# Performance work log

Measured on AMD Instinct MI355X. Metric: run time of the kernel, lower is better.

## Reference

```python
import jax, jax.numpy as jnp
import numpy as np

B, T, C, H, HS = 128, 256, 384, 6, 64
DFF = 4 * C
EPS = 1e-5


def layer_norm(x, g, b):
    mu = jnp.mean(x, axis=-1, keepdims=True)
    var = jnp.mean(jnp.square(x - mu), axis=-1, keepdims=True)
    return (x - mu) * jax.lax.rsqrt(var + EPS) * g + b


def setup_inputs() -> dict:
    key = jax.random.key(0)
    ks = jax.random.split(key, 12)
    s_in = 1.0 / np.sqrt(C)
    s_ff = 1.0 / np.sqrt(DFF)
    return {
        "x": jax.random.normal(ks[0], (B, T, C), jnp.float32),
        "Wq": jax.random.normal(ks[1], (H, C, HS), jnp.float32) * s_in,
        "Wk": jax.random.normal(ks[2], (H, C, HS), jnp.float32) * s_in,
        "Wv": jax.random.normal(ks[3], (H, C, HS), jnp.float32) * s_in,
        "Wo": jax.random.normal(ks[4], (C, C), jnp.float32) * s_in,
        "bo": jnp.zeros((C,), jnp.float32),
        "W1": jax.random.normal(ks[5], (C, DFF), jnp.float32) * s_in,
        "b1": jnp.zeros((DFF,), jnp.float32),
        "W2": jax.random.normal(ks[6], (DFF, C), jnp.float32) * s_ff,
        "b2": jnp.zeros((C,), jnp.float32),
        "g1": jnp.ones((C,), jnp.float32),
        "be1": jnp.zeros((C,), jnp.float32),
        "g2": jnp.ones((C,), jnp.float32),
        "be2": jnp.zeros((C,), jnp.float32),
    }


def reference(x, Wq, Wk, Wv, Wo, bo, W1, b1, W2, b2, g1, be1, g2, be2):
    # --- pre-norm causal multi-head self-attention (dropout = identity, eval mode) ---
    h = layer_norm(x, g1, be1)                      # (B,T,C)
    q = jnp.einsum('btc,hcd->bhtd', h, Wq)          # (B,H,T,HS)
    k = jnp.einsum('btc,hcd->bhtd', h, Wk)
    v = jnp.einsum('btc,hcd->bhtd', h, Wv)
    scale = HS ** -0.5
    wei = jnp.einsum('bhtd,bhsd->bhts', q, k) * scale   # (B,H,T,T)
    causal = jnp.tril(jnp.ones((T, T), bool))
    wei = jnp.where(causal, wei, -jnp.inf)
    wei = jax.nn.softmax(wei, axis=-1)
    attn = jnp.einsum('bhts,bhsd->bhtd', wei, v)         # (B,H,T,HS)
    attn = attn.transpose(0, 2, 1, 3).reshape(x.shape[0], x.shape[1], C)  # concat heads
    sa = attn @ Wo + bo
    x = x + sa
    # --- pre-norm FFN ---
    h2 = layer_norm(x, g2, be2)
    ff = jax.nn.relu(h2 @ W1 + b1) @ W2 + b2
    return x + ff
```

## Files before the change

### kernel.cpp

```cpp
#include <hip/hip_runtime.h>
#include <hip/hip_bf16.h>

#define BB   128
#define TT   256
#define CC   384
#define HH   6
#define HSZ  64
#define DFF  1536
#define EPSV 1e-5f
#define RPB  8
#define NTOK (BB * TT)
#define NQKV (3 * CC)

typedef __attribute__((ext_vector_type(8))) short  short8;
typedef __attribute__((ext_vector_type(4))) float  f32x4;
typedef __hip_bfloat16 bf16;

__device__ __forceinline__ void async_copy16(const bf16* g, bf16* l) {
    __builtin_amdgcn_global_load_lds(
        (const __attribute__((address_space(1))) void*)g,
        (__attribute__((address_space(3))) void*)l, 16, 0, 0);
}

__device__ __forceinline__ void block_reduce2(float& a, float& b, float* red) {
    #pragma unroll
    for (int off = 32; off > 0; off >>= 1) {
        a += __shfl_down(a, off, 64);
        b += __shfl_down(b, off, 64);
    }
    const int lane = threadIdx.x & 63;
    const int wid  = threadIdx.x >> 6;
    if (lane == 0) { red[wid * 2] = a; red[wid * 2 + 1] = b; }
    __syncthreads();
    if (threadIdx.x == 0) {
        float sa = 0.f, sb = 0.f;
        #pragma unroll
        for (int w = 0; w < 6; ++w) { sa += red[w * 2]; sb += red[w * 2 + 1]; }
        red[12] = sa; red[13] = sb;
    }
    __syncthreads();
    a = red[12]; b = red[13];
}

__global__ __launch_bounds__(CC) void ln_bf16_kernel(
        const float* __restrict__ x, const float* __restrict__ g,
        const float* __restrict__ be, bf16* __restrict__ y) {
    __shared__ float red[16];
    const int tid = threadIdx.x;
    const long row0 = (long)blockIdx.x * RPB;
    const float gg = g[tid], bb = be[tid];
    for (int r = 0; r < RPB; ++r) {
        float v = x[(row0 + r) * CC + tid];
        float s = v, sq = v * v;
        block_reduce2(s, sq, red);
        float mu  = s  * (1.0f / CC);
        float var = sq * (1.0f / CC) - mu * mu;
        float rs  = rsqrtf(var + EPSV);
        y[(row0 + r) * CC + tid] = __float2bfloat16((v - mu) * rs * gg + bb);
        __syncthreads();
    }
}

__global__ __launch_bounds__(256) void pack_weights(
        const float* __restrict__ Wq, const float* __restrict__ Wk,
        const float* __restrict__ Wv, const float* __restrict__ Wo,
        const float* __restrict__ W1, const float* __restrict__ W2,
        bf16* __restrict__ WcatT, bf16* __restrict__ WoT,
        bf16* __restrict__ W1T, bf16* __restrict__ W2T) {
    __shared__ float t[32][33];
    const int id = blockIdx.x;
    const float* in; bf16* out; int R, Cn, c0, r0;
    if (id < 432) {
        const int which = id / 144, rem = id % 144, h = rem / 24, tt = rem % 24;
        const float* W = (which == 0) ? Wq : ((which == 1) ? Wk : Wv);
        in = W + (long)h * CC * HSZ;  R = CC; Cn = HSZ;
        c0 = (tt % 2) * 32; r0 = (tt / 2) * 32;
        out = WcatT + ((long)which * CC + h * HSZ) * CC;
    } else if (id < 576) {
        const int i2 = id - 432;
        in = Wo; out = WoT; R = CC; Cn = CC;
        c0 = (i2 % 12) * 32; r0 = (i2 / 12) * 32;
    } else if (id < 1152) {
        const int i3 = id - 576;
        in = W1; out = W1T; R = CC; Cn = DFF;
        c0 = (i3 % 48) * 32; r0 = (i3 / 48) * 32;
    } else {
        const int i4 = id - 1152;
        in = W2; out = W2T; R = DFF; Cn = CC;
        c0 = (i4 % 12) * 32; r0 = (i4 / 12) * 32;
    }
    const int tid = threadIdx.x, tx = tid & 31, ty = tid >> 5;
    #pragma unroll
    for (int p = 0; p < 4; ++p)
        t[ty + p * 8][tx] = in[(long)(r0 + ty + p * 8) * Cn + c0 + tx];
    __syncthreads();
    #pragma unroll
    for (int p = 0; p < 4; ++p)
        out[(long)(c0 + ty + p * 8) * R + r0 + tx] = __float2bfloat16(t[tx][ty + p * 8]);
}

template<int K, int EPI>
__global__ __launch_bounds__(256) void gemm_bt(
        const bf16* __restrict__ A, const bf16* __restrict__ BT,
        const float* __restrict__ bias, const float* __restrict__ res,
        float* __restrict__ outF, bf16* __restrict__ outB, int N, int nby) {
    __shared__ bf16 As[2][128 * 32];
    __shared__ bf16 Bs[2][128 * 32];

    const int tid = threadIdx.x;

    const int hwid  = blockIdx.x;
    const int chunk = gridDim.x >> 3;
    const int e     = hwid & 7;
    const int s     = hwid >> 3;
    const int gx    = chunk / nby;
    const int bx    = e * gx + s / nby;
    const int by    = s - (s / nby) * nby;
    const int m0 = bx * 128;
    const int n0 = by * 128;

    const int ln   = tid & 63;
    const int wid  = tid >> 6;
    const int wm   = (wid & 1) * 64;
    const int wn   = (wid >> 1) * 64;
    const int fr   = ln & 15;
    const int quad = ln >> 4;
    const int slot = quad ^ ((fr >> 1) & 3);

    const int u0 = tid, u1 = tid + 256;
    const int r0c = u0 >> 2, g0 = (u0 & 3) ^ ((r0c >> 1) & 3);
    const int r1c = u1 >> 2, g1 = (u1 & 3) ^ ((r1c >> 1) & 3);
    const long ga0 = (long)r0c * K + g0 * 8;
    const long ga1 = (long)r1c * K + g1 * 8;
    const bf16* Ap  = A  + (long)m0 * K;
    const bf16* BTp = BT + (long)n0 * K;

    f32x4 acc[4][4];
    #pragma unroll
    for (int i = 0; i < 4; ++i)
        #pragma unroll
        for (int j = 0; j < 4; ++j)
            acc[i][j] = (f32x4){0.f, 0.f, 0.f, 0.f};

    constexpr int NT = K / 32;

    async_copy16(Ap  + ga0, As[0] + u0 * 8);
    async_copy16(Ap  + ga1, As[0] + u1 * 8);
    async_copy16(BTp + ga0, Bs[0] + u0 * 8);
    async_copy16(BTp + ga1, Bs[0] + u1 * 8);
    __syncthreads();

    int cur = 0;
    for (int t = 0; t < NT; ++t) {
        if (t + 1 < NT) {
            const int nxt = cur ^ 1;
            const long k0 = (long)(t + 1) * 32;
            async_copy16(Ap  + ga0 + k0, As[nxt] + u0 * 8);
            async_copy16(Ap  + ga1 + k0, As[nxt] + u1 * 8);
            async_copy16(BTp + ga0 + k0, Bs[nxt] + u0 * 8);
            async_copy16(BTp + ga1 + k0, Bs[nxt] + u1 * 8);
        }
        short8 af[4], bfr[4];
        #pragma unroll
        for (int i = 0; i < 4; ++i) {
            const int R = wm + i * 16 + fr;
            af[i] = *(const short8*)(As[cur] + R * 32 + slot * 8);
        }
        #pragma unroll
        for (int j = 0; j < 4; ++j) {
            const int R = wn + j * 16 + fr;
            bfr[j] = *(const short8*)(Bs[cur] + R * 32 + slot * 8);
        }
        #pragma unroll
        for (int i = 0; i < 4; ++i)
            #pragma unroll
            for (int j = 0; j < 4; ++j)
                acc[i][j] = __builtin_amdgcn_mfma_f32_16x16x32_bf16(
                    af[i], bfr[j], acc[i][j], 0, 0, 0);
        __syncthreads();
        cur ^= 1;
    }

    #pragma unroll
    for (int i = 0; i < 4; ++i) {
        #pragma unroll
        for (int j = 0; j < 4; ++j) {
            const int col = n0 + wn + j * 16 + fr;
            #pragma unroll
            for (int r = 0; r < 4; ++r) {
                const int row = m0 + wm + i * 16 + quad * 4 + r;
                const long idx = (long)row * N + col;
                float v = acc[i][j][r];
                if (EPI == 1) {
                    v = fmaxf(v + bias[col], 0.f);
                    outB[idx] = __float2bfloat16(v);
                } else if (EPI == 2) {
                    outF[idx] = v + bias[col] + res[idx];
                } else {
                    outB[idx] = __float2bfloat16(v);
                }
            }
        }
    }
}

struct alignas(8) bh4s { bf16 a, b, c, d; };

__global__ __launch_bounds__(256, 2) void attn_mfma_kernel(
        const bf16* __restrict__ qkv, bf16* __restrict__ ab) {
    __shared__ bf16 Kt[64][72];
    __shared__ bf16 Vt[64][72];
    __shared__ bf16 Pb[4][16][72];

    const int tid  = threadIdx.x;
    const int bh   = blockIdx.x;
    const int b    = bh / HH, h = bh % HH;
    const int w    = tid >> 6;
    const int ln   = tid & 63;
    const int ln15 = ln & 15;
    const int quad = ln >> 4;

    short8 qf[4][2];
    #pragma unroll
    for (int i = 0; i < 4; ++i) {
        const long tok = (long)b * TT + w * 16 + i * 64 + ln15;
        const bf16* p = qkv + tok * NQKV + h * HSZ + quad * 8;
        qf[i][0] = *(const short8*)p;
        qf[i][1] = *(const short8*)(p + 32);
    }

    f32x4 accO[4][4];
    float mrow[4][4], lrow[4][4];
    #pragma unroll
    for (int i = 0; i < 4; ++i) {
        #pragma unroll
        for (int j = 0; j < 4; ++j) accO[i][j] = (f32x4){0.f, 0.f, 0.f, 0.f};
        #pragma unroll
        for (int r = 0; r < 4; ++r) { mrow[i][r] = -1e30f; lrow[i][r] = 0.f; }
    }

    for (int sidx = 0; sidx < 4; ++sidx) {
        const int s0 = sidx * 64;
        __syncthreads();
        {
            const bf16* kg = qkv + (long)(b * TT + s0) * NQKV + CC + h * HSZ;
            #pragma unroll
            for (int it = 0; it < 2; ++it) {
                const int u = tid + it * 256;
                const int r = u >> 3, c = (u & 7) * 8;
                *(uint4*)&Kt[r][c] = *(const uint4*)(kg + (long)r * NQKV + c);
            }
            const bf16* vg = qkv + (long)(b * TT + s0) * NQKV + 2 * CC + h * HSZ;
            const int s = tid & 63;
            #pragma unroll
            for (int it = 0; it < 4; ++it) {
                const int dq = (tid >> 6) + it * 4;
                const bh4s vv = *(const bh4s*)(vg + (long)s * NQKV + dq * 4);
                Vt[dq * 4 + 0][s] = vv.a;
                Vt[dq * 4 + 1][s] = vv.b;
                Vt[dq * 4 + 2][s] = vv.c;
                Vt[dq * 4 + 3][s] = vv.d;
            }
        }
        __syncthreads();

        #pragma unroll
        for (int i = 0; i < 4; ++i) {
            if (i < sidx) continue;
            const int rb = w * 16 + i * 64;
            f32x4 S[4];
            #pragma unroll
            for (int jt = 0; jt < 4; ++jt) S[jt] = (f32x4){0.f, 0.f, 0.f, 0.f};
            #pragma unroll
            for (int ks = 0; ks < 2; ++ks) {
                #pragma unroll
                for (int jt = 0; jt < 4; ++jt) {
                    const short8 kf = *(const short8*)&Kt[jt * 16 + ln15][ks * 32 + quad * 8];
                    S[jt] = __builtin_amdgcn_mfma_f32_16x16x32_bf16(qf[i][ks], kf, S[jt], 0, 0, 0);
                }
            }
            float rmax[4];
            #pragma unroll
            for (int r = 0; r < 4; ++r) rmax[r] = -1e30f;
            #pragma unroll
            for (int jt = 0; jt < 4; ++jt) {
                #pragma unroll
                for (int r = 0; r < 4; ++r) {
                    float v = S[jt][r] * 0.125f;
                    if (i == sidx) {
                        const int col = s0 + jt * 16 + ln15;
                        const int row = rb + quad * 4 + r;
                        if (col > row) v = -1e30f;
                    }
                    S[jt][r] = v;
                    rmax[r] = fmaxf(rmax[r], v);
                }
            }
            #pragma unroll
            for (int off = 1; off < 16; off <<= 1)
                #pragma unroll
                for (int r = 0; r < 4; ++r)
                    rmax[r] = fmaxf(rmax[r], __shfl_xor(rmax[r], off, 64));

            float alpha[4], rsum[4];
            #pragma unroll
            for (int r = 0; r < 4; ++r) {
                const float mn = fmaxf(mrow[i][r], rmax[r]);
                alpha[r] = __expf(mrow[i][r] - mn);
                mrow[i][r] = mn;
                rsum[r] = 0.f;
            }
            #pragma unroll
            for (int jt = 0; jt < 4; ++jt)
                #pragma unroll
                for (int r = 0; r < 4; ++r) {
                    const float p = __expf(S[jt][r] - mrow[i][r]);
                    S[jt][r] = p;
                    rsum[r] += p;
                }
            #pragma unroll
            for (int off = 1; off < 16; off <<= 1)
                #pragma unroll
                for (int r = 0; r < 4; ++r)
                    rsum[r] += __shfl_xor(rsum[r], off, 64);
            #pragma unroll
            for (int r = 0; r < 4; ++r)
                lrow[i][r] = lrow[i][r] * alpha[r] + rsum[r];
            #pragma unroll
            for (int jt = 0; jt < 4; ++jt)
                #pragma unroll
                for (int r = 0; r < 4; ++r)
                    accO[i][jt][r] *= alpha[r];

            #pragma unroll
            for (int jt = 0; jt < 4; ++jt)
                #pragma unroll
                for (int r = 0; r < 4; ++r)
                    Pb[w][quad * 4 + r][jt * 16 + ln15] = __float2bfloat16(S[jt][r]);
            const short8 pf0 = *(const short8*)&Pb[w][ln15][quad * 8];
            const short8 pf1 = *(const short8*)&Pb[w][ln15][32 + quad * 8];
            #pragma unroll
            for (int jt = 0; jt < 4; ++jt) {
                const short8 vf0 = *(const short8*)&Vt[jt * 16 + ln15][quad * 8];
                const short8 vf1 = *(const short8*)&Vt[jt * 16 + ln15][32 + quad * 8];
                accO[i][jt] = __builtin_amdgcn_mfma_f32_16x16x32_bf16(pf0, vf0, accO[i][jt], 0, 0, 0);
                accO[i][jt] = __builtin_amdgcn_mfma_f32_16x16x32_bf16(pf1, vf1, accO[i][jt], 0, 0, 0);
            }
        }
    }

    #pragma unroll
    for (int i = 0; i < 4; ++i) {
        const int rb = w * 16 + i * 64;
        float inv[4];
        #pragma unroll
        for (int r = 0; r < 4; ++r) inv[r] = 1.0f / lrow[i][r];
        #pragma unroll
        for (int jt = 0; jt < 4; ++jt)
            #pragma unroll
            for (int r = 0; r < 4; ++r)
                Pb[w][quad * 4 + r][jt * 16 + ln15] = __float2bfloat16(accO[i][jt][r] * inv[r]);
        #pragma unroll
        for (int it = 0; it < 2; ++it) {
            const int u = ln + it * 64;
            const int row = u >> 3, ch = (u & 7) * 8;
            const long tok = (long)b * TT + rb + row;
            *(uint4*)(ab + tok * CC + h * HSZ + ch) = *(const uint4*)&Pb[w][row][ch];
        }
    }
}

extern "C" void kernel_launch(void* const* d_in, const int* in_sizes, int n_in,
                              void* d_out, int out_size, void* d_ws, size_t ws_size,
                              hipStream_t stream) {
    const float* x   = (const float*)d_in[0];
    const float* Wq  = (const float*)d_in[1];
    const float* Wk  = (const float*)d_in[2];
    const float* Wv  = (const float*)d_in[3];
    const float* Wo  = (const float*)d_in[4];
    const float* bo  = (const float*)d_in[5];
    const float* W1  = (const float*)d_in[6];
    const float* b1  = (const float*)d_in[7];
    const float* W2  = (const float*)d_in[8];
    const float* b2  = (const float*)d_in[9];
    const float* g1  = (const float*)d_in[10];
    const float* be1 = (const float*)d_in[11];
    const float* g2  = (const float*)d_in[12];
    const float* be2 = (const float*)d_in[13];

    float* out = (float*)d_out;
    char*  ws  = (char*)d_ws;

    const size_t qkvBytes = (size_t)NTOK * NQKV * 4;
    const size_t actOff   = (qkvBytes + 255) & ~(size_t)255;
    const size_t actBytes = (size_t)NTOK * CC * 2;
    size_t wOff = (actOff + actBytes + 255) & ~(size_t)255;

    bf16* qkvb = (bf16*)ws;
    bf16* ff1  = (bf16*)ws;
    bf16* actb = (bf16*)(ws + actOff);

    bf16* WcatT = (bf16*)(ws + wOff); wOff += (size_t)NQKV * CC * 2 + 256;
    bf16* WoT   = (bf16*)(ws + ((wOff + 255) & ~(size_t)255)); wOff = ((wOff + 255) & ~(size_t)255) + (size_t)CC * CC * 2;
    bf16* W1T   = (bf16*)(ws + ((wOff + 255) & ~(size_t)255)); wOff = ((wOff + 255) & ~(size_t)255) + (size_t)DFF * CC * 2;
    bf16* W2T   = (bf16*)(ws + ((wOff + 255) & ~(size_t)255));

    pack_weights<<<1728, 256, 0, stream>>>(Wq, Wk, Wv, Wo, W1, W2,
                                           WcatT, WoT, W1T, W2T);

    ln_bf16_kernel<<<NTOK / RPB, CC, 0, stream>>>(x, g1, be1, actb);
    gemm_bt<CC, 3><<<(NTOK / 128) * (NQKV / 128), 256, 0, stream>>>(
        actb, WcatT, nullptr, nullptr, nullptr, qkvb, NQKV, NQKV / 128);
    attn_mfma_kernel<<<BB * HH, 256, 0, stream>>>(qkvb, actb);
    gemm_bt<CC, 2><<<(NTOK / 128) * (CC / 128), 256, 0, stream>>>(
        actb, WoT, bo, x, out, nullptr, CC, CC / 128);

    ln_bf16_kernel<<<NTOK / RPB, CC, 0, stream>>>(out, g2, be2, actb);
    gemm_bt<CC, 1><<<(NTOK / 128) * (DFF / 128), 256, 0, stream>>>(
        actb, W1T, b1, nullptr, nullptr, ff1, DFF, DFF / 128);
    gemm_bt<DFF, 2><<<(NTOK / 128) * (CC / 128), 256, 0, stream>>>(
        ff1, W2T, b2, out, out, nullptr, CC, CC / 128);
}
```

Baseline: 432.2 us.

## Use 256x128 tiles, 8 waves and triple-buffered async LDS pipeline in GEMMs

```diff
diff --git a/kernel.cpp b/kernel.cpp
--- a/kernel.cpp
+++ b/kernel.cpp
@@ -15,6 +15,10 @@
 typedef __attribute__((ext_vector_type(8))) short  short8;
 typedef __attribute__((ext_vector_type(4))) float  f32x4;
 typedef __hip_bfloat16 bf16;
+
+#define WAITV(n) asm volatile("s_waitcnt vmcnt(" #n ")" ::: "memory")
+#define BAR      __builtin_amdgcn_s_barrier()
+#define SCHED    __builtin_amdgcn_sched_barrier(0)
 
 __device__ __forceinline__ void async_copy16(const bf16* g, bf16* l) {
     __builtin_amdgcn_global_load_lds(
@@ -100,12 +104,16 @@
 }
 
 template<int K, int EPI>
-__global__ __launch_bounds__(256) void gemm_bt(
+__global__ __launch_bounds__(512) void gemm8(
         const bf16* __restrict__ A, const bf16* __restrict__ BT,
         const float* __restrict__ bias, const float* __restrict__ res,
         float* __restrict__ outF, bf16* __restrict__ outB, int N, int nby) {
-    __shared__ bf16 As[2][128 * 32];
-    __shared__ bf16 Bs[2][128 * 32];
+    __shared__ bf16 A0[256 * 32];
+    __shared__ bf16 A1[256 * 32];
+    __shared__ bf16 A2[256 * 32];
+    __shared__ bf16 B0[128 * 32];
+    __shared__ bf16 B1[128 * 32];
+    __shared__ bf16 B2[128 * 32];
 
     const int tid = threadIdx.x;
 
@@ -116,75 +124,81 @@
     const int gx    = chunk / nby;
     const int bx    = e * gx + s / nby;
     const int by    = s - (s / nby) * nby;
-    const int m0 = bx * 128;
+    const int m0 = bx * 256;
     const int n0 = by * 128;
 
     const int ln   = tid & 63;
     const int wid  = tid >> 6;
-    const int wm   = (wid & 1) * 64;
-    const int wn   = (wid >> 1) * 64;
+    const int wm   = (wid & 1) * 128;
+    const int wn   = (wid >> 1) * 32;
     const int fr   = ln & 15;
     const int quad = ln >> 4;
     const int slot = quad ^ ((fr >> 1) & 3);
 
-    const int u0 = tid, u1 = tid + 256;
-    const int r0c = u0 >> 2, g0 = (u0 & 3) ^ ((r0c >> 1) & 3);
-    const int r1c = u1 >> 2, g1 = (u1 & 3) ^ ((r1c >> 1) & 3);
-    const long ga0 = (long)r0c * K + g0 * 8;
-    const long ga1 = (long)r1c * K + g1 * 8;
     const bf16* Ap  = A  + (long)m0 * K;
     const bf16* BTp = BT + (long)n0 * K;
 
-    f32x4 acc[4][4];
-    #pragma unroll
-    for (int i = 0; i < 4; ++i)
-        #pragma unroll
-        for (int j = 0; j < 4; ++j)
+    f32x4 acc[8][2];
+    #pragma unroll
+    for (int i = 0; i < 8; ++i)
+        #pragma unroll
+        for (int j = 0; j < 2; ++j)
             acc[i][j] = (f32x4){0.f, 0.f, 0.f, 0.f};
 
     constexpr int NT = K / 32;
-
-    async_copy16(Ap  + ga0, As[0] + u0 * 8);
-    async_copy16(Ap  + ga1, As[0] + u1 * 8);
-    async_copy16(BTp + ga0, Bs[0] + u0 * 8);
-    async_copy16(BTp + ga1, Bs[0] + u1 * 8);
-    __syncthreads();
-
-    int cur = 0;
-    for (int t = 0; t < NT; ++t) {
-        if (t + 1 < NT) {
-            const int nxt = cur ^ 1;
-            const long k0 = (long)(t + 1) * 32;
-            async_copy16(Ap  + ga0 + k0, As[nxt] + u0 * 8);
-            async_copy16(Ap  + ga1 + k0, As[nxt] + u1 * 8);
-            async_copy16(BTp + ga0 + k0, Bs[nxt] + u0 * 8);
-            async_copy16(BTp + ga1 + k0, Bs[nxt] + u1 * 8);
-        }
-        short8 af[4], bfr[4];
-        #pragma unroll
-        for (int i = 0; i < 4; ++i) {
-            const int R = wm + i * 16 + fr;
-            af[i] = *(const short8*)(As[cur] + R * 32 + slot * 8);
-        }
-        #pragma unroll
-        for (int j = 0; j < 4; ++j) {
-            const int R = wn + j * 16 + fr;
-            bfr[j] = *(const short8*)(Bs[cur] + R * 32 + slot * 8);
-        }
-        #pragma unroll
-        for (int i = 0; i < 4; ++i)
-            #pragma unroll
-            for (int j = 0; j < 4; ++j)
+    static_assert(NT % 3 == 0, "3-buffer rotation requires NT % 3 == 0");
+
+    auto stageT = [&](long k0, bf16* Ad, bf16* Bd) {
+        #pragma unroll
+        for (int p = 0; p < 2; ++p) {
+            const int u = tid + p * 512;
+            const int row = u >> 2;
+            const int cc  = (u & 3) ^ ((row >> 1) & 3);
+            async_copy16(Ap + (long)row * K + k0 + cc * 8, Ad + u * 8);
+        }
+        {
+            const int u = tid;
+            const int row = u >> 2;
+            const int cc  = (u & 3) ^ ((row >> 1) & 3);
+            async_copy16(BTp + (long)row * K + k0 + cc * 8, Bd + u * 8);
+        }
+    };
+
+    auto phase = [&](int t, const bf16* Ar, const bf16* Br, bf16* As_, bf16* Bs_) {
+        if (t + 1 < NT) { WAITV(3); } else { WAITV(0); }
+        BAR;
+        SCHED;
+        short8 af[8], bfr[2];
+        #pragma unroll
+        for (int i = 0; i < 8; ++i)
+            af[i] = *(const short8*)(Ar + (wm + i * 16 + fr) * 32 + slot * 8);
+        #pragma unroll
+        for (int j = 0; j < 2; ++j)
+            bfr[j] = *(const short8*)(Br + (wn + j * 16 + fr) * 32 + slot * 8);
+        if (t + 2 < NT) stageT((long)(t + 2) * 32, As_, Bs_);
+        __builtin_amdgcn_s_setprio(1);
+        #pragma unroll
+        for (int i = 0; i < 8; ++i)
+            #pragma unroll
+            for (int j = 0; j < 2; ++j)
                 acc[i][j] = __builtin_amdgcn_mfma_f32_16x16x32_bf16(
                     af[i], bfr[j], acc[i][j], 0, 0, 0);
-        __syncthreads();
-        cur ^= 1;
-    }
-
-    #pragma unroll
-    for (int i = 0; i < 4; ++i) {
-        #pragma unroll
-        for (int j = 0; j < 4; ++j) {
+        __builtin_amdgcn_s_setprio(0);
+    };
+
+    stageT(0,  A0, B0);
+    stageT(32, A1, B1);
+
+    for (int t = 0; t < NT; t += 3) {
+        phase(t,     A0, B0, A2, B2);
+        phase(t + 1, A1, B1, A0, B0);
+        phase(t + 2, A2, B2, A1, B1);
+    }
+
+    #pragma unroll
+    for (int i = 0; i < 8; ++i) {
+        #pragma unroll
+        for (int j = 0; j < 2; ++j) {
             const int col = n0 + wn + j * 16 + fr;
             #pragma unroll
             for (int r = 0; r < 4; ++r) {
@@ -409,15 +423,15 @@
                                            WcatT, WoT, W1T, W2T);
 
     ln_bf16_kernel<<<NTOK / RPB, CC, 0, stream>>>(x, g1, be1, actb);
-    gemm_bt<CC, 3><<<(NTOK / 128) * (NQKV / 128), 256, 0, stream>>>(
+    gemm8<CC, 3><<<(NTOK / 256) * (NQKV / 128), 512, 0, stream>>>(
         actb, WcatT, nullptr, nullptr, nullptr, qkvb, NQKV, NQKV / 128);
     attn_mfma_kernel<<<BB * HH, 256, 0, stream>>>(qkvb, actb);
-    gemm_bt<CC, 2><<<(NTOK / 128) * (CC / 128), 256, 0, stream>>>(
+    gemm8<CC, 2><<<(NTOK / 256) * (CC / 128), 512, 0, stream>>>(
         actb, WoT, bo, x, out, nullptr, CC, CC / 128);
 
     ln_bf16_kernel<<<NTOK / RPB, CC, 0, stream>>>(out, g2, be2, actb);
-    gemm_bt<CC, 1><<<(NTOK / 128) * (DFF / 128), 256, 0, stream>>>(
+    gemm8<CC, 1><<<(NTOK / 256) * (DFF / 128), 512, 0, stream>>>(
         actb, W1T, b1, nullptr, nullptr, ff1, DFF, DFF / 128);
-    gemm_bt<DFF, 2><<<(NTOK / 128) * (CC / 128), 256, 0, stream>>>(
+    gemm8<DFF, 2><<<(NTOK / 256) * (CC / 128), 512, 0, stream>>>(
         ff1, W2T, b2, out, out, nullptr, CC, CC / 128);
 }
```

Measured after the change: 427.2 us. About the same (-1.2%).
